# Kernel optimization log

Hardware: AMD Instinct MI355X
Metric: run time of the kernel (lower is better)

Reference implementation:

```python
import jax, jax.numpy as jnp
import numpy as np

B = 8192   # batch
N = 1024   # input feature dim
D = 64     # rotation dimension
K = D * (D - 1) // 2  # 2016 upper-triangular entries


def setup_inputs() -> dict:
    key = jax.random.key(0)
    k1, k2 = jax.random.split(key, 2)
    x = jax.random.normal(k1, (B, N), dtype=jnp.float32)
    # nn.Linear(N, K) parameters (kaiming-uniform-ish scale)
    W = jax.random.normal(k2, (K, N), dtype=jnp.float32) / np.float32(np.sqrt(N))
    b = jnp.zeros((K,), dtype=jnp.float32)
    return {"x": x, "W": W, "b": b}


def _skew_expm(A):
    # A is real skew-symmetric => iA is Hermitian: iA = V diag(w) V^H, w real.
    # Hence expm(A) = V diag(exp(-i w)) V^H, which is real orthogonal.
    # Mathematically identical to torch.linalg.matrix_exp(A).
    w, V = jnp.linalg.eigh(1j * A)              # complex64 eigh, batched
    R = jnp.einsum('bij,bj,bkj->bik', V, jnp.exp(-1j * w), V.conj())
    return jnp.real(R)


def reference(x, W, b):
    v = jax.nn.silu(x) @ W.T + b                # (B, K)
    iu, ju = jnp.triu_indices(D, k=1)           # strict upper triangle
    A = jnp.zeros((x.shape[0], D, D), v.dtype)
    A = A.at[:, iu, ju].set(v)
    A = A.at[:, ju, iu].set(-v)                 # skew-symmetric
    return _skew_expm(A)                        # (B, D, D)
```

## Files before the change

kernel.cpp:

```cpp
#include <hip/hip_runtime.h>
#include <hip/hip_bf16.h>
#include <hip/hip_fp16.h>
#include <math.h>

#define BB 8192
#define NF 1024
#define KKc 2016
#define DD 64

typedef unsigned short u16;
typedef __attribute__((ext_vector_type(4))) float f32x4;
typedef __attribute__((ext_vector_type(4))) unsigned int u32x4;
typedef __attribute__((ext_vector_type(8))) short s16x8;
typedef __attribute__((ext_vector_type(8))) _Float16 f16x8;
typedef __attribute__((ext_vector_type(8))) unsigned short u16x8;

union BF2U { __hip_bfloat162 b; unsigned u; };
union H2U { __half2 h; unsigned u; };
union FragX { u16x8 u; s16x8 s; u32x4 d; };
union F16U { s16x8 s; f16x8 h; };

__device__ __forceinline__ unsigned pk_hi(float a, float b, float& fa, float& fb) {
  BF2U r; r.b = __float22bfloat162_rn(make_float2(a, b));
  float2 f = __bfloat1622float2(r.b);
  fa = f.x; fb = f.y;
  return r.u;
}
__device__ __forceinline__ unsigned pk(float a, float b) {
  BF2U r; r.b = __float22bfloat162_rn(make_float2(a, b));
  return r.u;
}
__device__ __forceinline__ unsigned pkh(float a, float b) {
  H2U r; r.h = __float22half2_rn(make_float2(a, b));
  return r.u;
}

__device__ __forceinline__ void split4(const float t0, const float t1, const float t2,
                                       const float t3, uint2& h, uint2& l) {
  float f0, f1, f2, f3;
  h.x = pk_hi(t0, t1, f0, f1);
  h.y = pk_hi(t2, t3, f2, f3);
  l.x = pk(t0 - f0, t1 - f1);
  l.y = pk(t2 - f2, t3 - f3);
}

__global__ __launch_bounds__(256)
void silu_f16_kernel(const float* __restrict__ x, u16* __restrict__ xf) {
  const int idx = blockIdx.x * 256 + threadIdx.x;
  float4 vv = ((const float4*)x)[idx];
  float a[4] = {vv.x, vv.y, vv.z, vv.w};
#pragma unroll
  for (int i = 0; i < 4; i++) a[i] = a[i] / (1.f + __expf(-a[i]));
  uint2 o;
  o.x = pkh(a[0], a[1]);
  o.y = pkh(a[2], a[3]);
  ((uint2*)xf)[idx] = o;
}

__global__ __launch_bounds__(256)
void w_f16_kernel(const float* __restrict__ W, u16* __restrict__ wfp) {
  const int idx = blockIdx.x * 256 + threadIdx.x;
  const int row = idx >> 8;
  float4 vv = make_float4(0.f, 0.f, 0.f, 0.f);
  if (row < KKc) vv = ((const float4*)W)[idx];
  uint2 o;
  o.x = pkh(vv.x, vv.y);
  o.y = pkh(vv.z, vv.w);
  ((uint2*)wfp)[idx] = o;
}

typedef __attribute__((address_space(1))) const unsigned int gu32;
typedef __attribute__((address_space(3))) unsigned int lu32;

__device__ __forceinline__ void gload_lds16(const void* g, void* l) {
  __builtin_amdgcn_global_load_lds((gu32*)g, (lu32*)l, 16, 0, 0);
}

__device__ __forceinline__ s16x8 frag_row32(const u16* T, int row, int kc) {
  const int c = kc ^ ((row >> 1) & 3);
  return *(const s16x8*)(T + row * 32 + c * 8);
}

__global__ __launch_bounds__(256, 4)
void gemm_f16_kernel(const u16* __restrict__ xf, const u16* __restrict__ wfp,
                     const float* __restrict__ bias, float* __restrict__ v) {
  __shared__ __align__(16) u16 Af[128 * 32];
  __shared__ __align__(16) u16 Bf[128 * 32];
  const int tid = threadIdx.x;
  const int l = tid & 63, w = tid >> 6;
  const int wi = w >> 1, wj = w & 1;
  const int lin = (blockIdx.x & 7) * 128 + (blockIdx.x >> 3);
  const int n0 = (lin & 15) * 128;
  const int m0 = (lin >> 4) * 128;
  const int kc = l >> 4, lr = l & 15;

  const u16* P = (w < 2) ? xf : wfp;
  u16* T = (w < 2) ? Af : Bf;
  const int row0 = ((w < 2) ? m0 : n0) + (w & 1) * 64;
  u16* Th = T + (w & 1) * 2048;

  f32x4 acc[4][4];
  const f32x4 zz = {0.f, 0.f, 0.f, 0.f};
#pragma unroll
  for (int a = 0; a < 4; a++)
#pragma unroll
    for (int b = 0; b < 4; b++) acc[a][b] = zz;

  for (int k0 = 0; k0 < NF; k0 += 32) {
#pragma unroll
    for (int c4 = 0; c4 < 4; c4++) {
      const int slot = c4 * 64 + l;
      const int r = slot >> 2;
      const int c = (slot & 3) ^ ((r >> 1) & 3);
      gload_lds16(P + (size_t)(row0 + r) * NF + k0 + c * 8, Th + c4 * 512);
    }
    __syncthreads();

    F16U fa[4], fb[4];
#pragma unroll
    for (int a = 0; a < 4; a++) fa[a].s = frag_row32(Af, wi * 64 + a * 16 + lr, kc);
#pragma unroll
    for (int b = 0; b < 4; b++) fb[b].s = frag_row32(Bf, wj * 64 + b * 16 + lr, kc);
#pragma unroll
    for (int b = 0; b < 4; b++)
#pragma unroll
      for (int a = 0; a < 4; a++)
        acc[a][b] = __builtin_amdgcn_mfma_f32_16x16x32_f16(fa[a].h, fb[b].h, acc[a][b], 0, 0, 0);
    __syncthreads();
  }

  const int grp = l >> 4;
#pragma unroll
  for (int b = 0; b < 4; b++) {
    const int n = n0 + wj * 64 + b * 16 + lr;
    if (n < KKc) {
      const float bb = bias[n];
#pragma unroll
      for (int a = 0; a < 4; a++) {
        const int mbase = m0 + wi * 64 + a * 16 + grp * 4;
#pragma unroll
        for (int i = 0; i < 4; i++)
          v[(size_t)(mbase + i) * KKc + n] = acc[a][b][i] + bb;
      }
    }
  }
}

#define BM 128
#define BN 128
#define BKr 16
#define XST 132

__global__ __launch_bounds__(256, 2)
void gemm_silu_kernel(const float* __restrict__ x, const float* __restrict__ W,
                      const float* __restrict__ bias, float* __restrict__ v) {
  __shared__ float xs[BKr * XST];
  __shared__ float wl[BKr * XST];
  const int tid = threadIdx.x;
  const int tx = tid & 15, ty = tid >> 4;
  const int c0g = blockIdx.x * BN;
  const int m0 = blockIdx.y * BM;
  const int lrow = tid >> 2;
  const int lu = (tid & 3) << 2;

  float acc[2][2][4][4];
#pragma unroll
  for (int a = 0; a < 2; a++)
#pragma unroll
    for (int b = 0; b < 2; b++)
#pragma unroll
      for (int i = 0; i < 4; i++)
#pragma unroll
        for (int j = 0; j < 4; j++) acc[a][b][i][j] = 0.f;

  for (int n0 = 0; n0 < NF; n0 += BKr) {
#pragma unroll
    for (int p = 0; p < 2; p++) {
      const int row = lrow + 64 * p;
      float4 xv = *(const float4*)(x + (size_t)(m0 + row) * NF + n0 + lu);
      float xa[4] = {xv.x, xv.y, xv.z, xv.w};
#pragma unroll
      for (int u = 0; u < 4; u++) {
        const float val = xa[u];
        xs[(lu + u) * XST + row] = val / (1.f + __expf(-val));
      }
      const int wr = c0g + row;
      float4 wv = make_float4(0.f, 0.f, 0.f, 0.f);
      if (wr < KKc) wv = *(const float4*)(W + (size_t)wr * NF + n0 + lu);
      float wa[4] = {wv.x, wv.y, wv.z, wv.w};
#pragma unroll
      for (int u = 0; u < 4; u++) wl[(lu + u) * XST + row] = wa[u];
    }
    __syncthreads();
#pragma unroll
    for (int k0 = 0; k0 < BKr; k0 += 4) {
#pragma unroll
      for (int kk = 0; kk < 4; kk++) {
        const float* xr = xs + (k0 + kk) * XST;
        const float* wr_ = wl + (k0 + kk) * XST;
        float4 t;
        t = *(const float4*)(xr + 4 * ty);       float a0[4] = {t.x, t.y, t.z, t.w};
        t = *(const float4*)(xr + 64 + 4 * ty);  float a1[4] = {t.x, t.y, t.z, t.w};
        t = *(const float4*)(wr_ + 4 * tx);      float b0[4] = {t.x, t.y, t.z, t.w};
        t = *(const float4*)(wr_ + 64 + 4 * tx); float b1[4] = {t.x, t.y, t.z, t.w};
#pragma unroll
        for (int i = 0; i < 4; i++)
#pragma unroll
          for (int j = 0; j < 4; j++) {
            acc[0][0][i][j] = fmaf(a0[i], b0[j], acc[0][0][i][j]);
            acc[0][1][i][j] = fmaf(a0[i], b1[j], acc[0][1][i][j]);
            acc[1][0][i][j] = fmaf(a1[i], b0[j], acc[1][0][i][j]);
            acc[1][1][i][j] = fmaf(a1[i], b1[j], acc[1][1][i][j]);
          }
      }
    }
    __syncthreads();
  }
#pragma unroll
  for (int rb = 0; rb < 2; rb++)
#pragma unroll
    for (int ii = 0; ii < 4; ii++) {
      const int row = m0 + rb * 64 + 4 * ty + ii;
#pragma unroll
      for (int cb = 0; cb < 2; cb++) {
        const int c = c0g + cb * 64 + 4 * tx;
        if (c < KKc) {
          float4 bb = *(const float4*)(bias + c);
          float4 o;
          o.x = acc[rb][cb][ii][0] + bb.x;
          o.y = acc[rb][cb][ii][1] + bb.y;
          o.z = acc[rb][cb][ii][2] + bb.z;
          o.w = acc[rb][cb][ii][3] + bb.w;
          *(float4*)(v + (size_t)row * KKc + c) = o;
        }
      }
    }
}


__device__ __forceinline__ s16x8 fragld(const u16* P, int row, int chunk) {
  return *(const s16x8*)(P + ((row << 6) | ((chunk ^ (row & 7)) << 3)));
}

__device__ __forceinline__ s16x8 fneg(s16x8 f) {
  FragX x; x.s = f;
  x.d ^= (u32x4){0x80008000u, 0x80008000u, 0x80008000u, 0x80008000u};
  return x.s;
}

template<int NPASS, bool NEGB>
__device__ __forceinline__ void mat_mm(const u16* APh, const u16* APl,
                                       const u16* BPh, const u16* BPl,
                                       f32x4 acc[2][2], int wi, int wj, int g, int lr) {
#pragma unroll
  for (int kb = 0; kb < 2; kb++) {
    const int ch = (kb << 2) | g;
    s16x8 bh[2], bl[2];
#pragma unroll
    for (int b = 0; b < 2; b++) {
      const int n = wj * 32 + b * 16 + lr;
      bh[b] = fragld(BPh, n, ch);
      if (NEGB) bh[b] = fneg(bh[b]);
      if (NPASS == 3) {
        bl[b] = fragld(BPl, n, ch);
        if (NEGB) bl[b] = fneg(bl[b]);
      }
    }
#pragma unroll
    for (int a = 0; a < 2; a++) {
      const int r = wi * 32 + a * 16 + lr;
      const s16x8 ah = fragld(APh, r, ch);
      s16x8 al;
      if (NPASS == 3) al = fragld(APl, r, ch);
#pragma unroll
      for (int b = 0; b < 2; b++) {
        acc[a][b] = __builtin_amdgcn_mfma_f32_16x16x32_bf16(ah, bh[b], acc[a][b], 0, 0, 0);
        if (NPASS == 3) {
          acc[a][b] = __builtin_amdgcn_mfma_f32_16x16x32_bf16(ah, bl[b], acc[a][b], 0, 0, 0);
          acc[a][b] = __builtin_amdgcn_mfma_f32_16x16x32_bf16(al, bh[b], acc[a][b], 0, 0, 0);
        }
      }
    }
  }
}

__device__ __forceinline__ void mat_mm1h(const u16* AP, const u16* BP,
                                         f32x4 acc[2][2], int wi, int wj, int g, int lr) {
#pragma unroll
  for (int kb = 0; kb < 2; kb++) {
    const int ch = (kb << 2) | g;
    F16U bh[2];
#pragma unroll
    for (int b = 0; b < 2; b++) bh[b].s = fragld(BP, wj * 32 + b * 16 + lr, ch);
#pragma unroll
    for (int a = 0; a < 2; a++) {
      F16U ah; ah.s = fragld(AP, wi * 32 + a * 16 + lr, ch);
#pragma unroll
      for (int b = 0; b < 2; b++)
        acc[a][b] = __builtin_amdgcn_mfma_f32_16x16x32_f16(ah.h, bh[b].h, acc[a][b], 0, 0, 0);
    }
  }
}

__device__ __forceinline__ void mat_mm68h(const u16* X4p, const u16* X2p,
                                          f32x4 acc6[2][2], f32x4 acc8[2][2],
                                          int wi, int wj, int g, int lr) {
#pragma unroll
  for (int kb = 0; kb < 2; kb++) {
    const int ch = (kb << 2) | g;
    F16U b2[2], b4[2];
#pragma unroll
    for (int b = 0; b < 2; b++) {
      const int n = wj * 32 + b * 16 + lr;
      b2[b].s = fragld(X2p, n, ch);
      b4[b].s = fragld(X4p, n, ch);
    }
#pragma unroll
    for (int a = 0; a < 2; a++) {
      F16U ah; ah.s = fragld(X4p, wi * 32 + a * 16 + lr, ch);
#pragma unroll
      for (int b = 0; b < 2; b++) {
        acc6[a][b] = __builtin_amdgcn_mfma_f32_16x16x32_f16(ah.h, b2[b].h, acc6[a][b], 0, 0, 0);
        acc8[a][b] = __builtin_amdgcn_mfma_f32_16x16x32_f16(ah.h, b4[b].h, acc8[a][b], 0, 0, 0);
      }
    }
  }
}

__device__ __forceinline__ void pack_col(u16* Ch, u16* Cl, const f32x4 acc[2][2],
                                         int wi, int wj, int g, int lr) {
#pragma unroll
  for (int a = 0; a < 2; a++) {
    const int r0 = wi * 32 + a * 16 + g * 4;
#pragma unroll
    for (int b = 0; b < 2; b++) {
      const int c = wj * 32 + b * 16 + lr;
      uint2 h, l;
      split4(acc[a][b][0], acc[a][b][1], acc[a][b][2], acc[a][b][3], h, l);
      const int ad = (c << 6) | (((((r0 >> 3)) ^ (c & 7)) << 3) | (r0 & 7));
      *(uint2*)(Ch + ad) = h;
      *(uint2*)(Cl + ad) = l;
    }
  }
}

__device__ __forceinline__ void pack_colh(u16* C, const f32x4 acc[2][2], float sc,
                                          int wi, int wj, int g, int lr) {
#pragma unroll
  for (int a = 0; a < 2; a++) {
    const int r0 = wi * 32 + a * 16 + g * 4;
#pragma unroll
    for (int b = 0; b < 2; b++) {
      const int c = wj * 32 + b * 16 + lr;
      uint2 h;
      h.x = pkh(sc * acc[a][b][0], sc * acc[a][b][1]);
      h.y = pkh(sc * acc[a][b][2], sc * acc[a][b][3]);
      const int ad = (c << 6) | (((((r0 >> 3)) ^ (c & 7)) << 3) | (r0 & 7));
      *(uint2*)(C + ad) = h;
    }
  }
}

__device__ __forceinline__ void pack_dualh(u16* Rrow, u16* Rcol, const f32x4 acc[2][2],
                                           int wi, int wj, int g, int lr) {
#pragma unroll
  for (int a = 0; a < 2; a++) {
    const int r0 = wi * 32 + a * 16 + g * 4;
#pragma unroll
    for (int b = 0; b < 2; b++) {
      const int c = wj * 32 + b * 16 + lr;
      uint2 h;
      h.x = pkh(acc[a][b][0], acc[a][b][1]);
      h.y = pkh(acc[a][b][2], acc[a][b][3]);
      const int adc = (c << 6) | (((((r0 >> 3)) ^ (c & 7)) << 3) | (r0 & 7));
      *(uint2*)(Rcol + adc) = h;
      const u16 hv[4] = {(u16)h.x, (u16)(h.x >> 16), (u16)h.y, (u16)(h.y >> 16)};
#pragma unroll
      for (int i = 0; i < 4; i++) {
        const int r = r0 + i;
        const int adr = (r << 6) | ((((c >> 3) ^ (r & 7)) << 3) | (c & 7));
        Rrow[adr] = hv[i];
      }
    }
  }
}

__global__ __launch_bounds__(256, 5)
void expm_kernel(const float* __restrict__ v, float* __restrict__ out) {
  __shared__ __align__(16) u16 PAh[4096], PAl[4096];
  __shared__ __align__(16) u16 PF2[4096], PF4[4096];
  const int tid = threadIdx.x;
  const int bid = blockIdx.x;
  const int l = tid & 63, w = tid >> 6;
  const int g = l >> 4, lr = l & 15;
  const int wi = w >> 1, wj = w & 1;

  {
    float* vb = (float*)PF2;
    const float* vr = v + (size_t)bid * KKc;
    for (int i = tid; i < KKc; i += 256) vb[i] = vr[i];
  }
  __syncthreads();

  {
    const float* vb = (const float*)PF2;
    const int arow = tid >> 2, q = tid & 3;
    float va[16];
#pragma unroll
    for (int j = 0; j < 16; j++) {
      const int c = q * 16 + j;
      float val = 0.f;
      if (arow < c)      val =  vb[(arow * (127 - arow)) / 2 + c - arow - 1];
      else if (arow > c) val = -vb[(c * (127 - c)) / 2 + arow - c - 1];
      va[j] = val;
    }
#pragma unroll
    for (int cc = 0; cc < 2; cc++) {
      const int ch = 2 * q + cc;
      const int ad = (arow << 6) | ((ch ^ (arow & 7)) << 3);
      unsigned hw[4], lw[4];
#pragma unroll
      for (int p = 0; p < 4; p++) {
        const float a = va[cc * 8 + 2 * p], b = va[cc * 8 + 2 * p + 1];
        float fa, fb;
        hw[p] = pk_hi(a, b, fa, fb);
        lw[p] = pk(a - fa, b - fb);
      }
      *(u32x4*)(PAh + ad) = (u32x4){hw[0], hw[1], hw[2], hw[3]};
      *(u32x4*)(PAl + ad) = (u32x4){lw[0], lw[1], lw[2], lw[3]};
    }
  }
  __syncthreads();

  const f32x4 zz = {0.f, 0.f, 0.f, 0.f};
  f32x4 acc[2][2];

  acc[0][0] = zz; acc[0][1] = zz; acc[1][0] = zz; acc[1][1] = zz;
  mat_mm<3, true>(PAh, PAl, PAh, PAl, acc, wi, wj, g, lr);
  f32x4 rA2[2][2];
  rA2[0][0] = acc[0][0]; rA2[0][1] = acc[0][1]; rA2[1][0] = acc[1][0]; rA2[1][1] = acc[1][1];

  {
    float fs = 0.f;
#pragma unroll
    for (int a = 0; a < 2; a++)
#pragma unroll
      for (int b = 0; b < 2; b++)
#pragma unroll
        for (int i = 0; i < 4; i++) fs = fmaf(rA2[a][b][i], rA2[a][b][i], fs);
#pragma unroll
    for (int k = 1; k < 64; k <<= 1) fs += __shfl_xor(fs, k, 64);
    if (l == 0) ((float*)PF4)[w] = fs;
  }
  __syncthreads();
  const float* redA = (const float*)PF4;
  const float nf4 = redA[0] + redA[1] + redA[2] + redA[3];
  int s = 0;
  if (nf4 > 16.f) {
    s = (int)ceilf(0.25f * log2f(nf4) - 1.0f);
    if (s < 0) s = 0;
    if (s > 15) s = 15;
  }
  const float t = exp2f(-(float)s);
  const float t2 = t * t;

  pack_colh(PF2, rA2, t2, wi, wj, g, lr);
  __syncthreads();

  acc[0][0] = zz; acc[0][1] = zz; acc[1][0] = zz; acc[1][1] = zz;
  mat_mm1h(PF2, PF2, acc, wi, wj, g, lr);
  f32x4 rE[2][2], rS3[2][2];
#pragma unroll
  for (int a = 0; a < 2; a++)
#pragma unroll
    for (int b = 0; b < 2; b++)
#pragma unroll
      for (int i = 0; i < 4; i++) {
        const int row = wi * 32 + a * 16 + g * 4 + i;
        const int col = wj * 32 + b * 16 + lr;
        const float dg = (row == col) ? 1.f : 0.f;
        rE[a][b][i]  = dg + (0.5f * t2) * rA2[a][b][i] + (1.f / 24.f) * acc[a][b][i];
        rS3[a][b][i] = t * dg + (t * t2 / 6.f) * rA2[a][b][i]
                             + (t / 120.f) * acc[a][b][i];
      }
  pack_colh(PF4, acc, 1.f, wi, wj, g, lr);
  __syncthreads();

  f32x4 acc6[2][2], acc8[2][2];
  acc6[0][0] = zz; acc6[0][1] = zz; acc6[1][0] = zz; acc6[1][1] = zz;
  acc8[0][0] = zz; acc8[0][1] = zz; acc8[1][0] = zz; acc8[1][1] = zz;
  mat_mm68h(PF4, PF2, acc6, acc8, wi, wj, g, lr);
#pragma unroll
  for (int a = 0; a < 2; a++)
#pragma unroll
    for (int b = 0; b < 2; b++)
#pragma unroll
      for (int i = 0; i < 4; i++) {
        rE[a][b][i]  += (1.f / 720.f) * acc6[a][b][i] + (1.f / 40320.f) * acc8[a][b][i];
        rS3[a][b][i] += (t / 5040.f) * acc6[a][b][i] + (t / 362880.f) * acc8[a][b][i];
      }
  __syncthreads();

  pack_col(PF2, PF4, rS3, wi, wj, g, lr);
  __syncthreads();

  acc[0][0] = rE[0][0]; acc[0][1] = rE[0][1]; acc[1][0] = rE[1][0]; acc[1][1] = rE[1][1];
  mat_mm<3, false>(PAh, PAl, PF2, PF4, acc, wi, wj, g, lr);
  __syncthreads();

  for (int it = 0; it < s; it++) {
    u16* Rrow = (it & 1) ? PF2 : PAl;
    u16* Rcol = (it & 1) ? PF4 : PAh;
    pack_dualh(Rrow, Rcol, acc, wi, wj, g, lr);
    __syncthreads();
    acc[0][0] = zz; acc[0][1] = zz; acc[1][0] = zz; acc[1][1] = zz;
    mat_mm1h(Rrow, Rcol, acc, wi, wj, g, lr);
  }

  float* ob = out + (size_t)bid * 4096;
#pragma unroll
  for (int a = 0; a < 2; a++)
#pragma unroll
    for (int b = 0; b < 2; b++)
#pragma unroll
      for (int i = 0; i < 4; i++) {
        const int row = wi * 32 + a * 16 + g * 4 + i;
        const int col = wj * 32 + b * 16 + lr;
        ob[row * 64 + col] = acc[a][b][i];
      }
}

extern "C" void kernel_launch(void* const* d_in, const int* in_sizes, int n_in,
                              void* d_out, int out_size, void* d_ws, size_t ws_size,
                              hipStream_t stream) {
  const float* x = (const float*)d_in[0];
  const float* W = (const float*)d_in[1];
  const float* bias = (const float*)d_in[2];
  float* out = (float*)d_out;
  char* ws = (char*)d_ws;
  float* v = (float*)ws;

  const size_t V_BYTES  = (size_t)BB * KKc * 4;
  const size_t XF_ELEMS = (size_t)BB * NF;
  const size_t WF_ELEMS = (size_t)2048 * NF;
  const size_t NEED = V_BYTES + (XF_ELEMS + WF_ELEMS) * 2;

  if (ws_size >= NEED) {
    u16* xf = (u16*)(ws + V_BYTES);
    u16* wfp = xf + XF_ELEMS;
    silu_f16_kernel<<<dim3(BB * NF / 4 / 256), dim3(256), 0, stream>>>(x, xf);
    w_f16_kernel<<<dim3(2048 * NF / 4 / 256), dim3(256), 0, stream>>>(W, wfp);
    gemm_f16_kernel<<<dim3(1024), dim3(256), 0, stream>>>(xf, wfp, bias, v);
  } else {
    dim3 g1((KKc + BN - 1) / BN, BB / BM);
    gemm_silu_kernel<<<g1, dim3(256), 0, stream>>>(x, W, bias, v);
  }
  expm_kernel<<<dim3(BB), dim3(256), 0, stream>>>(v, out);
}
```

Measured before the change: 191.9 us.

## Choose scaling from A^8 norm estimate and compute A^2 in single-pass fp16

A^2 is now computed with one fp16 MFMA pass instead of the three-pass bf16 hi/lo split. A^4 is formed early, and its Frobenius norm (written to global scratch as per-wave partials) sets the scaling exponent, which can be smaller than the bound from the A^2 norm. This should mean fewer squaring iterations. The Taylor terms are rescaled by powers of r, the A^6 and A^8 products are issued as separate fp16 matmuls, and the occupancy hint drops from 5 to 4. Risks: lower accuracy in A^2, and the global-memory reduction reuses workspace that the fp16 GEMM path also uses (xf), after that GEMM has already consumed it.

```diff
diff --git a/kernel.cpp b/kernel.cpp
--- a/kernel.cpp
+++ b/kernel.cpp
@@ -17,7 +17,6 @@
 
 union BF2U { __hip_bfloat162 b; unsigned u; };
 union H2U { __half2 h; unsigned u; };
-union FragX { u16x8 u; s16x8 s; u32x4 d; };
 union F16U { s16x8 s; f16x8 h; };
 
 __device__ __forceinline__ unsigned pk_hi(float a, float b, float& fa, float& fb) {
@@ -242,16 +241,9 @@
   return *(const s16x8*)(P + ((row << 6) | ((chunk ^ (row & 7)) << 3)));
 }
 
-__device__ __forceinline__ s16x8 fneg(s16x8 f) {
-  FragX x; x.s = f;
-  x.d ^= (u32x4){0x80008000u, 0x80008000u, 0x80008000u, 0x80008000u};
-  return x.s;
-}
-
-template<int NPASS, bool NEGB>
-__device__ __forceinline__ void mat_mm(const u16* APh, const u16* APl,
-                                       const u16* BPh, const u16* BPl,
-                                       f32x4 acc[2][2], int wi, int wj, int g, int lr) {
+__device__ __forceinline__ void mat_mm3(const u16* APh, const u16* APl,
+                                        const u16* BPh, const u16* BPl,
+                                        f32x4 acc[2][2], int wi, int wj, int g, int lr) {
 #pragma unroll
   for (int kb = 0; kb < 2; kb++) {
     const int ch = (kb << 2) | g;
@@ -260,25 +252,18 @@
     for (int b = 0; b < 2; b++) {
       const int n = wj * 32 + b * 16 + lr;
       bh[b] = fragld(BPh, n, ch);
-      if (NEGB) bh[b] = fneg(bh[b]);
-      if (NPASS == 3) {
-        bl[b] = fragld(BPl, n, ch);
-        if (NEGB) bl[b] = fneg(bl[b]);
-      }
+      bl[b] = fragld(BPl, n, ch);
     }
 #pragma unroll
     for (int a = 0; a < 2; a++) {
       const int r = wi * 32 + a * 16 + lr;
       const s16x8 ah = fragld(APh, r, ch);
-      s16x8 al;
-      if (NPASS == 3) al = fragld(APl, r, ch);
+      const s16x8 al = fragld(APl, r, ch);
 #pragma unroll
       for (int b = 0; b < 2; b++) {
         acc[a][b] = __builtin_amdgcn_mfma_f32_16x16x32_bf16(ah, bh[b], acc[a][b], 0, 0, 0);
-        if (NPASS == 3) {
-          acc[a][b] = __builtin_amdgcn_mfma_f32_16x16x32_bf16(ah, bl[b], acc[a][b], 0, 0, 0);
-          acc[a][b] = __builtin_amdgcn_mfma_f32_16x16x32_bf16(al, bh[b], acc[a][b], 0, 0, 0);
-        }
+        acc[a][b] = __builtin_amdgcn_mfma_f32_16x16x32_bf16(ah, bl[b], acc[a][b], 0, 0, 0);
+        acc[a][b] = __builtin_amdgcn_mfma_f32_16x16x32_bf16(al, bh[b], acc[a][b], 0, 0, 0);
       }
     }
   }
@@ -298,31 +283,6 @@
 #pragma unroll
       for (int b = 0; b < 2; b++)
         acc[a][b] = __builtin_amdgcn_mfma_f32_16x16x32_f16(ah.h, bh[b].h, acc[a][b], 0, 0, 0);
-    }
-  }
-}
-
-__device__ __forceinline__ void mat_mm68h(const u16* X4p, const u16* X2p,
-                                          f32x4 acc6[2][2], f32x4 acc8[2][2],
-                                          int wi, int wj, int g, int lr) {
-#pragma unroll
-  for (int kb = 0; kb < 2; kb++) {
-    const int ch = (kb << 2) | g;
-    F16U b2[2], b4[2];
-#pragma unroll
-    for (int b = 0; b < 2; b++) {
-      const int n = wj * 32 + b * 16 + lr;
-      b2[b].s = fragld(X2p, n, ch);
-      b4[b].s = fragld(X4p, n, ch);
-    }
-#pragma unroll
-    for (int a = 0; a < 2; a++) {
-      F16U ah; ah.s = fragld(X4p, wi * 32 + a * 16 + lr, ch);
-#pragma unroll
-      for (int b = 0; b < 2; b++) {
-        acc6[a][b] = __builtin_amdgcn_mfma_f32_16x16x32_f16(ah.h, b2[b].h, acc6[a][b], 0, 0, 0);
-        acc8[a][b] = __builtin_amdgcn_mfma_f32_16x16x32_f16(ah.h, b4[b].h, acc8[a][b], 0, 0, 0);
-      }
     }
   }
 }
@@ -385,8 +345,9 @@
   }
 }
 
-__global__ __launch_bounds__(256, 5)
-void expm_kernel(const float* __restrict__ v, float* __restrict__ out) {
+__global__ __launch_bounds__(256, 4)
+void expm_kernel(const float* __restrict__ v, float* __restrict__ out,
+                 float* __restrict__ redg) {
   __shared__ __align__(16) u16 PAh[4096], PAl[4096];
   __shared__ __align__(16) u16 PF2[4096], PF4[4096];
   const int tid = threadIdx.x;
@@ -418,16 +379,18 @@
     for (int cc = 0; cc < 2; cc++) {
       const int ch = 2 * q + cc;
       const int ad = (arow << 6) | ((ch ^ (arow & 7)) << 3);
-      unsigned hw[4], lw[4];
+      unsigned hw[4], lw[4], fw[4];
 #pragma unroll
       for (int p = 0; p < 4; p++) {
         const float a = va[cc * 8 + 2 * p], b = va[cc * 8 + 2 * p + 1];
         float fa, fb;
         hw[p] = pk_hi(a, b, fa, fb);
         lw[p] = pk(a - fa, b - fb);
+        fw[p] = pkh(a, b);
       }
       *(u32x4*)(PAh + ad) = (u32x4){hw[0], hw[1], hw[2], hw[3]};
       *(u32x4*)(PAl + ad) = (u32x4){lw[0], lw[1], lw[2], lw[3]};
+      *(u32x4*)(PF4 + ad) = (u32x4){fw[0], fw[1], fw[2], fw[3]};
     }
   }
   __syncthreads();
@@ -436,10 +399,9 @@
   f32x4 acc[2][2];
 
   acc[0][0] = zz; acc[0][1] = zz; acc[1][0] = zz; acc[1][1] = zz;
-  mat_mm<3, true>(PAh, PAl, PAh, PAl, acc, wi, wj, g, lr);
-  f32x4 rA2[2][2];
-  rA2[0][0] = acc[0][0]; rA2[0][1] = acc[0][1]; rA2[1][0] = acc[1][0]; rA2[1][1] = acc[1][1];
-
+  mat_mm1h(PF4, PF4, acc, wi, wj, g, lr);
+  f32x4 rM[2][2];
+  rM[0][0] = acc[0][0]; rM[0][1] = acc[0][1]; rM[1][0] = acc[1][0]; rM[1][1] = acc[1][1];
   {
     float fs = 0.f;
 #pragma unroll
@@ -447,28 +409,56 @@
 #pragma unroll
       for (int b = 0; b < 2; b++)
 #pragma unroll
-        for (int i = 0; i < 4; i++) fs = fmaf(rA2[a][b][i], rA2[a][b][i], fs);
+        for (int i = 0; i < 4; i++) fs = fmaf(rM[a][b][i], rM[a][b][i], fs);
 #pragma unroll
     for (int k = 1; k < 64; k <<= 1) fs += __shfl_xor(fs, k, 64);
-    if (l == 0) ((float*)PF4)[w] = fs;
-  }
-  __syncthreads();
-  const float* redA = (const float*)PF4;
+    if (l == 0) ((float*)PF2)[w] = fs;
+  }
+  __syncthreads();
+
+  const float* redA = (const float*)PF2;
   const float nf4 = redA[0] + redA[1] + redA[2] + redA[3];
+  int s0 = 0;
+  if (nf4 > 1.f) {
+    s0 = (int)ceilf(0.25f * log2f(nf4));
+    if (s0 < 0) s0 = 0;
+    if (s0 > 15) s0 = 15;
+  }
+  const float t0 = exp2f(-(float)s0);
+
+  pack_colh(PF4, rM, -(t0 * t0), wi, wj, g, lr);
+  __syncthreads();
+
+  acc[0][0] = zz; acc[0][1] = zz; acc[1][0] = zz; acc[1][1] = zz;
+  mat_mm1h(PF4, PF4, acc, wi, wj, g, lr);
+  {
+    float fs = 0.f;
+#pragma unroll
+    for (int a = 0; a < 2; a++)
+#pragma unroll
+      for (int b = 0; b < 2; b++)
+#pragma unroll
+        for (int i = 0; i < 4; i++) fs = fmaf(acc[a][b][i], acc[a][b][i], fs);
+#pragma unroll
+    for (int k = 1; k < 64; k <<= 1) fs += __shfl_xor(fs, k, 64);
+    if (l == 0) redg[bid * 4 + w] = fs;
+  }
+  pack_colh(PF2, acc, 1.f, wi, wj, g, lr);
+  __syncthreads();
+
+  const float nf8 = redg[bid * 4 + 0] + redg[bid * 4 + 1]
+                  + redg[bid * 4 + 2] + redg[bid * 4 + 3];
   int s = 0;
-  if (nf4 > 16.f) {
-    s = (int)ceilf(0.25f * log2f(nf4) - 1.0f);
+  if (nf8 > 1e-30f) {
+    s = (int)ceilf(0.125f * log2f(nf8) + (float)s0 - 1.0f);
     if (s < 0) s = 0;
     if (s > 15) s = 15;
   }
   const float t = exp2f(-(float)s);
+  const float r = exp2f((float)(s0 - s));
+  const float r2 = r * r, r4 = r2 * r2, r6 = r4 * r2, r8 = r4 * r4;
   const float t2 = t * t;
 
-  pack_colh(PF2, rA2, t2, wi, wj, g, lr);
-  __syncthreads();
-
-  acc[0][0] = zz; acc[0][1] = zz; acc[1][0] = zz; acc[1][1] = zz;
-  mat_mm1h(PF2, PF2, acc, wi, wj, g, lr);
   f32x4 rE[2][2], rS3[2][2];
 #pragma unroll
   for (int a = 0; a < 2; a++)
@@ -479,33 +469,40 @@
         const int row = wi * 32 + a * 16 + g * 4 + i;
         const int col = wj * 32 + b * 16 + lr;
         const float dg = (row == col) ? 1.f : 0.f;
-        rE[a][b][i]  = dg + (0.5f * t2) * rA2[a][b][i] + (1.f / 24.f) * acc[a][b][i];
-        rS3[a][b][i] = t * dg + (t * t2 / 6.f) * rA2[a][b][i]
-                             + (t / 120.f) * acc[a][b][i];
-      }
-  pack_colh(PF4, acc, 1.f, wi, wj, g, lr);
-  __syncthreads();
-
-  f32x4 acc6[2][2], acc8[2][2];
-  acc6[0][0] = zz; acc6[0][1] = zz; acc6[1][0] = zz; acc6[1][1] = zz;
-  acc8[0][0] = zz; acc8[0][1] = zz; acc8[1][0] = zz; acc8[1][1] = zz;
-  mat_mm68h(PF4, PF2, acc6, acc8, wi, wj, g, lr);
+        rE[a][b][i]  = dg - (0.5f * t2) * rM[a][b][i] + (r4 / 24.f) * acc[a][b][i];
+        rS3[a][b][i] = t * dg - (t * t2 / 6.f) * rM[a][b][i]
+                             + (t * r4 / 120.f) * acc[a][b][i];
+      }
+
+  acc[0][0] = zz; acc[0][1] = zz; acc[1][0] = zz; acc[1][1] = zz;
+  mat_mm1h(PF2, PF4, acc, wi, wj, g, lr);
 #pragma unroll
   for (int a = 0; a < 2; a++)
 #pragma unroll
     for (int b = 0; b < 2; b++)
 #pragma unroll
       for (int i = 0; i < 4; i++) {
-        rE[a][b][i]  += (1.f / 720.f) * acc6[a][b][i] + (1.f / 40320.f) * acc8[a][b][i];
-        rS3[a][b][i] += (t / 5040.f) * acc6[a][b][i] + (t / 362880.f) * acc8[a][b][i];
-      }
-  __syncthreads();
-
-  pack_col(PF2, PF4, rS3, wi, wj, g, lr);
+        rE[a][b][i]  += (r6 / 720.f) * acc[a][b][i];
+        rS3[a][b][i] += (t * r6 / 5040.f) * acc[a][b][i];
+      }
+  acc[0][0] = zz; acc[0][1] = zz; acc[1][0] = zz; acc[1][1] = zz;
+  mat_mm1h(PF2, PF2, acc, wi, wj, g, lr);
+#pragma unroll
+  for (int a = 0; a < 2; a++)
+#pragma unroll
+    for (int b = 0; b < 2; b++)
+#pragma unroll
+      for (int i = 0; i < 4; i++) {
+        rE[a][b][i]  += (r8 / 40320.f) * acc[a][b][i];
+        rS3[a][b][i] += (t * r8 / 362880.f) * acc[a][b][i];
+      }
+  __syncthreads();
+
+  pack_col(PF4, PF2, rS3, wi, wj, g, lr);
   __syncthreads();
 
   acc[0][0] = rE[0][0]; acc[0][1] = rE[0][1]; acc[1][0] = rE[1][0]; acc[1][1] = rE[1][1];
-  mat_mm<3, false>(PAh, PAl, PF2, PF4, acc, wi, wj, g, lr);
+  mat_mm3(PAh, PAl, PF4, PF2, acc, wi, wj, g, lr);
   __syncthreads();
 
   for (int it = 0; it < s; it++) {
@@ -544,6 +541,7 @@
   const size_t XF_ELEMS = (size_t)BB * NF;
   const size_t WF_ELEMS = (size_t)2048 * NF;
   const size_t NEED = V_BYTES + (XF_ELEMS + WF_ELEMS) * 2;
+  float* redg = (float*)(ws + V_BYTES);
 
   if (ws_size >= NEED) {
     u16* xf = (u16*)(ws + V_BYTES);
@@ -555,5 +553,5 @@
     dim3 g1((KKc + BN - 1) / BN, BB / BM);
     gemm_silu_kernel<<<g1, dim3(256), 0, stream>>>(x, W, bias, v);
   }
-  expm_kernel<<<dim3(BB), dim3(256), 0, stream>>>(v, out);
-}
+  expm_kernel<<<dim3(BB), dim3(256), 0, stream>>>(v, out, redg);
+}
```

Result: faster. 167.1 us (-12.9%).
